# Optimization experiments

Measured on AMD Instinct MI355X. Metric: run time of the kernel, lower is better.

## Reference

```python
import jax, jax.numpy as jnp
import numpy as np

N_NODES = 50000


def gcn_conv(x, W, b, row, col, num_nodes):
    """PyG-style GCNConv: out = D^{-1/2}(A+I)D^{-1/2} (x @ W) + b.

    row/col already include self-loops. x: [N, Fin], W: [Fin, Fout].
    """
    h = x @ W  # [N, Fout]
    deg = jax.ops.segment_sum(jnp.ones_like(col, dtype=h.dtype), col,
                              num_segments=num_nodes)  # in-degree incl. self-loop
    dinv = jnp.where(deg > 0, jax.lax.rsqrt(deg), 0.0)
    norm = dinv[row] * dinv[col]  # [E]
    msgs = h[row] * norm[:, None]  # gather + scale, [E, Fout]
    out = jax.ops.segment_sum(msgs, col, num_segments=num_nodes)  # scatter-add
    return out + b


def setup_inputs() -> dict:
    key = jax.random.key(0)
    k1, k2, k3, k4 = jax.random.split(key, 4)
    Fin, Fh, Fout = 128, 128, 64
    E = 800000
    x = jax.random.normal(k1, (N_NODES, Fin), dtype=jnp.float32)
    edge_index = jax.random.randint(k2, (2, E), 0, N_NODES, dtype=jnp.int64)
    # Glorot-ish init for weights
    W1 = jax.random.normal(k3, (Fin, Fh), dtype=jnp.float32) / np.sqrt(Fin)
    b1 = jnp.zeros((Fh,), dtype=jnp.float32)
    W2 = jax.random.normal(k4, (Fh, Fout), dtype=jnp.float32) / np.sqrt(Fh)
    b2 = jnp.zeros((Fout,), dtype=jnp.float32)
    return {"x": x, "edge_index": edge_index, "W1": W1, "b1": b1,
            "W2": W2, "b2": b2}


def reference(x, edge_index, W1, b1, W2, b2):
    n = x.shape[0]
    # add self-loops once (shared by both conv layers)
    loops = jnp.arange(n, dtype=edge_index.dtype)
    row = jnp.concatenate([edge_index[0], loops])
    col = jnp.concatenate([edge_index[1], loops])
    h = jax.nn.relu(gcn_conv(x, W1, b1, row, col, n))
    # dropout(p=0.5) is identity in eval mode (self.training == False)
    return gcn_conv(h, W2, b2, row, col, n)
```

## Files before the change

kernel.cpp:

```cpp
#include <hip/hip_runtime.h>


constexpr int KD = 128;
constexpr int CHUNK = 2048;
constexpr int BCAP = 6144;

using short8  = __attribute__((ext_vector_type(8))) short;
using float4v = __attribute__((ext_vector_type(4))) float;
using uint4v  = __attribute__((ext_vector_type(4))) unsigned int;


__device__ __forceinline__ unsigned short f2bf(float f) {
    unsigned int u = __float_as_uint(f);
    u = (u + 0x7fffu + ((u >> 16) & 1u)) >> 16;
    return (unsigned short)u;
}

__device__ __forceinline__ float2 bfpair(unsigned int u) {
    float2 f;
    f.x = __uint_as_float(u << 16);
    f.y = __uint_as_float(u & 0xffff0000u);
    return f;
}

__device__ __forceinline__ unsigned int packbf(float x, float y) {
    return (unsigned int)f2bf(x) | ((unsigned int)f2bf(y) << 16);
}

__device__ __forceinline__ void bfsplit(float x, unsigned short& h, unsigned short& l) {
    h = f2bf(x);
    float fh = __uint_as_float((unsigned int)h << 16);
    l = f2bf(x - fh);
}

__global__ __launch_bounds__(256) void scatter_setup(
        const int* __restrict__ row, const int* __restrict__ col,
        int* gcur, unsigned int* __restrict__ bpack, int E, int NBS,
        const float* __restrict__ W1, unsigned short* __restrict__ Wth1,
        unsigned short* __restrict__ Wtl1,
        const float* __restrict__ W2, unsigned short* __restrict__ Wth2,
        unsigned short* __restrict__ Wtl2) {
    __shared__ int lh[256];
    __shared__ int lbase[256];

    if ((int)blockIdx.x >= NBS) {
        int id = ((int)blockIdx.x - NBS) * 256 + threadIdx.x;
        unsigned short h, l;
        if (id < 16384) {
            int k = id >> 7, n = id & 127;
            bfsplit(W1[id], h, l);
            Wth1[n * KD + k] = h;
            Wtl1[n * KD + k] = l;
        } else {
            int id2 = id - 16384;
            int k = id2 >> 6, n = id2 & 63;
            bfsplit(W2[id2], h, l);
            Wth2[n * KD + k] = h;
            Wtl2[n * KD + k] = l;
        }
        return;
    }

    lh[threadIdx.x] = 0;
    __syncthreads();
    int base = (int)blockIdx.x * CHUNK;
#pragma unroll
    for (int r = 0; r < CHUNK / 256; ++r) {
        int e = base + r * 256 + threadIdx.x;
        if (e < E) atomicAdd(&lh[col[e] >> 8], 1);
    }
    __syncthreads();
    int c0 = lh[threadIdx.x];
    lbase[threadIdx.x] = c0 ? (threadIdx.x * BCAP + atomicAdd(&gcur[threadIdx.x], c0)) : 0;
    __syncthreads();
    lh[threadIdx.x] = 0;
    __syncthreads();
#pragma unroll
    for (int r = 0; r < CHUNK / 256; ++r) {
        int e = base + r * 256 + threadIdx.x;
        if (e < E) {
            int c = col[e];
            int b = c >> 8;
            int slot = lbase[b] + atomicAdd(&lh[b], 1);
            bpack[slot] = ((unsigned int)row[e] << 16) | (unsigned int)c;
        }
    }
}

__global__ __launch_bounds__(256) void csr_and_gemm1(
        const unsigned int* __restrict__ bpack, const int* __restrict__ gcur,
        int* __restrict__ rowptr, float* __restrict__ dinv,
        unsigned short* __restrict__ srow, int N, int E, int NBUCKET,
        const float* __restrict__ X,
        const unsigned short* __restrict__ Wth,
        const unsigned short* __restrict__ Wtl,
        unsigned short* __restrict__ G) {
    __shared__ int s[256];
    __shared__ int lh[256];
    __shared__ int lcur[256];
    __shared__ int sh_bstart;

    if ((int)blockIdx.x < NBUCKET) {
        int b = blockIdx.x;
        int t = threadIdx.x;
        int cntb = gcur[t];
        s[t] = cntb;
        __syncthreads();
        for (int off = 1; off < 256; off <<= 1) {
            int tv = (t >= off) ? s[t - off] : 0;
            __syncthreads();
            s[t] += tv;
            __syncthreads();
        }
        if (t == b) sh_bstart = s[t] - cntb;
        if (b == 0 && t == 0) rowptr[N] = E;
        lh[t] = 0;
        __syncthreads();
        int bstart = sh_bstart;
        int nE = gcur[b];
        int base = b * BCAP;
        for (int i = t; i < nE; i += 256)
            atomicAdd(&lh[bpack[base + i] & 255], 1);
        __syncthreads();
        int v = lh[t];
        s[t] = v;
        __syncthreads();
        for (int off = 1; off < 256; off <<= 1) {
            int tv = (t >= off) ? s[t - off] : 0;
            __syncthreads();
            s[t] += tv;
            __syncthreads();
        }
        int myStart = bstart + s[t] - v;
        int node = (b << 8) + t;
        if (node < N) {
            rowptr[node] = myStart;
            dinv[node] = rsqrtf(1.0f + (float)v);
        }
        lcur[t] = myStart;
        __syncthreads();
        for (int i = t; i < nE; i += 256) {
            unsigned int p = bpack[base + i];
            int slot = atomicAdd(&lcur[p & 255], 1);
            srow[slot] = (unsigned short)(p >> 16);
        }
    } else {
        constexpr int FOUT = 128, NT = 8;
        int wave = threadIdx.x >> 6;
        int lane = threadIdx.x & 63;
        int row0 = (((int)blockIdx.x - NBUCKET) * 4 + wave) * 16;
        if (row0 >= N) return;
        int m = lane & 15;
        int quad = lane >> 4;

        float4v acc[NT];
#pragma unroll
        for (int ct = 0; ct < NT; ++ct) acc[ct] = (float4v){0.f, 0.f, 0.f, 0.f};

        const float* xrow = X + (size_t)(row0 + m) * KD + quad * 8;

#pragma unroll
        for (int ks = 0; ks < 4; ++ks) {
            float4 xa = *(const float4*)(xrow + ks * 32);
            float4 xb = *(const float4*)(xrow + ks * 32 + 4);
            float xs[8] = {xa.x, xa.y, xa.z, xa.w, xb.x, xb.y, xb.z, xb.w};
            short8 ah, al;
#pragma unroll
            for (int j = 0; j < 8; ++j) {
                unsigned short h, l;
                bfsplit(xs[j], h, l);
                ah[j] = (short)h;
                al[j] = (short)l;
            }
            int koff = ks * 32 + quad * 8;
#pragma unroll
            for (int ct = 0; ct < NT; ++ct) {
                short8 bh = *(const short8*)(Wth + (size_t)(ct * 16 + m) * KD + koff);
                short8 bl = *(const short8*)(Wtl + (size_t)(ct * 16 + m) * KD + koff);
                acc[ct] = __builtin_amdgcn_mfma_f32_16x16x32_bf16(ah, bh, acc[ct], 0, 0, 0);
                acc[ct] = __builtin_amdgcn_mfma_f32_16x16x32_bf16(al, bh, acc[ct], 0, 0, 0);
                acc[ct] = __builtin_amdgcn_mfma_f32_16x16x32_bf16(ah, bl, acc[ct], 0, 0, 0);
            }
        }

#pragma unroll
        for (int r = 0; r < 4; ++r) {
            int row = row0 + quad * 4 + r;
#pragma unroll
            for (int ct = 0; ct < NT; ++ct) {
                G[(size_t)row * FOUT + ct * 16 + m] = f2bf(acc[ct][r]);
            }
        }
    }
}

__global__ __launch_bounds__(256) void gather128_gemm2(
        const int* __restrict__ rowptr,
        const unsigned short* __restrict__ srow,
        const unsigned int* __restrict__ G,
        const float* __restrict__ dinv,
        const float* __restrict__ bias,
        const unsigned short* __restrict__ Wth,
        const unsigned short* __restrict__ Wtl,
        unsigned short* __restrict__ G2,
        int N, int E) {
    __shared__ unsigned int lhs[16 * 64];
    __shared__ float ldinv[16];

    int lane = threadIdx.x & 63;
    int l16 = threadIdx.x & 15;
    int q = threadIdx.x >> 4;
    int node = (int)blockIdx.x * 16 + q;
    bool valid = node < N;
    int nc = valid ? node : 0;
    int beg = rowptr[nc];
    int end = rowptr[nc + 1];
    int deg = valid ? (end - beg) : 0;
    float dn = dinv[nc];
    if (l16 == 0) ldinv[q] = dn;

    const uint4v* Gv = (const uint4v*)G;

    uint4v s0 = Gv[(size_t)nc * 16 + l16];
    float ac[8];
    {
        float2 v0 = bfpair(s0[0]), v1 = bfpair(s0[1]);
        float2 v2 = bfpair(s0[2]), v3 = bfpair(s0[3]);
        ac[0] = v0.x * dn; ac[1] = v0.y * dn;
        ac[2] = v1.x * dn; ac[3] = v1.y * dn;
        ac[4] = v2.x * dn; ac[5] = v2.y * dn;
        ac[6] = v3.x * dn; ac[7] = v3.y * dn;
    }

    int dm = max(deg, __shfl_xor(deg, 16));
    dm = max(dm, __shfl_xor(dm, 32));

    for (int w = 0; w < dm; w += 16) {
        int li = w + l16;
        li = (li < deg) ? li : (deg > 0 ? deg - 1 : 0);
        li += beg;
        li = (li < E) ? li : (E - 1);
        int rv = (int)srow[li];
        float dv = dinv[rv];
        int lim = dm - w;
        for (int g = 0; g < 16 && g < lim; g += 4) {
            uint4v u[4];
            float dr[4];
#pragma unroll
            for (int j = 0; j < 4; ++j) {
                int src = (lane & 48) | (g + j);
                int r = __shfl(rv, src);
                dr[j] = __shfl(dv, src);
                u[j] = Gv[(size_t)r * 16 + l16];
            }
            float s[8] = {0.f, 0.f, 0.f, 0.f, 0.f, 0.f, 0.f, 0.f};
#pragma unroll
            for (int j = 0; j < 4; ++j) {
                bool ok = (w + g + j) < deg;
#pragma unroll
                for (int c = 0; c < 4; ++c) {
                    unsigned int uv = ok ? u[j][c] : 0u;
                    float2 v = bfpair(uv);
                    s[2 * c]     = fmaf(dr[j], v.x, s[2 * c]);
                    s[2 * c + 1] = fmaf(dr[j], v.y, s[2 * c + 1]);
                }
            }
#pragma unroll
            for (int c = 0; c < 8; ++c) ac[c] += s[c];
        }
    }

    {
        float4 bv0 = ((const float4*)bias)[l16 * 2];
        float4 bv1 = ((const float4*)bias)[l16 * 2 + 1];
        float o[8];
        o[0] = ac[0] * dn + bv0.x; o[1] = ac[1] * dn + bv0.y;
        o[2] = ac[2] * dn + bv0.z; o[3] = ac[3] * dn + bv0.w;
        o[4] = ac[4] * dn + bv1.x; o[5] = ac[5] * dn + bv1.y;
        o[6] = ac[6] * dn + bv1.z; o[7] = ac[7] * dn + bv1.w;
#pragma unroll
        for (int c = 0; c < 8; ++c) o[c] = fmaxf(o[c], 0.f);
        int lb = q * 64 + l16 * 4;
        lhs[lb + 0] = packbf(o[0], o[1]);
        lhs[lb + 1] = packbf(o[2], o[3]);
        lhs[lb + 2] = packbf(o[4], o[5]);
        lhs[lb + 3] = packbf(o[6], o[7]);
    }
    __syncthreads();

    int ct = threadIdx.x >> 6;
    int m = lane & 15;
    int quad = lane >> 4;

    float4v acc = (float4v){0.f, 0.f, 0.f, 0.f};
#pragma unroll
    for (int ks = 0; ks < 4; ++ks) {
        short8 a = *(const short8*)&lhs[m * 64 + ks * 16 + quad * 4];
        int koff = ks * 32 + quad * 8;
        short8 bh = *(const short8*)(Wth + (size_t)(ct * 16 + m) * KD + koff);
        short8 bl = *(const short8*)(Wtl + (size_t)(ct * 16 + m) * KD + koff);
        acc = __builtin_amdgcn_mfma_f32_16x16x32_bf16(a, bh, acc, 0, 0, 0);
        acc = __builtin_amdgcn_mfma_f32_16x16x32_bf16(a, bl, acc, 0, 0, 0);
    }

#pragma unroll
    for (int r = 0; r < 4; ++r) {
        int rr = quad * 4 + r;
        int gnode = (int)blockIdx.x * 16 + rr;
        if (gnode < N) {
            G2[(size_t)gnode * 64 + ct * 16 + m] = f2bf(acc[r] * ldinv[rr]);
        }
    }
}

template <bool RELU>
__global__ __launch_bounds__(256) void gather64(const int* __restrict__ rowptr,
                                                const unsigned short* __restrict__ srow,
                                                const unsigned int* __restrict__ G,
                                                const float* __restrict__ dinv,
                                                const float* __restrict__ bias,
                                                float* __restrict__ O, int N, int E) {
    int tid = blockIdx.x * 256 + (int)threadIdx.x;
    int node = tid >> 4;
    int lane = threadIdx.x & 63;
    int l16 = lane & 15;
    bool valid = node < N;
    int nc = valid ? node : (N - 1);
    int beg = rowptr[nc];
    int end = rowptr[nc + 1];
    int deg = valid ? (end - beg) : 0;

    uint2 s0 = ((const uint2*)G)[(size_t)nc * 16 + l16];
    float2 p0 = bfpair(s0.x), p1 = bfpair(s0.y);
    float ax = p0.x, ay = p0.y, az = p1.x, aw = p1.y;

    int dm = max(deg, __shfl_xor(deg, 16));
    dm = max(dm, __shfl_xor(dm, 32));

    for (int w = 0; w < dm; w += 16) {
        int li = w + l16;
        li = (li < deg) ? li : (deg > 0 ? deg - 1 : 0);
        li += beg;
        li = (li < E) ? li : (E - 1);
        int rv = (int)srow[li];
        int lim = dm - w;
        for (int g = 0; g < 16 && g < lim; g += 8) {
            uint2 u[8];
#pragma unroll
            for (int j = 0; j < 8; ++j) {
                int src = (lane & 48) | (g + j);
                int r = __shfl(rv, src);
                u[j] = ((const uint2*)G)[(size_t)r * 16 + l16];
            }
            float sx = 0.f, sy = 0.f, sz = 0.f, sw = 0.f;
#pragma unroll
            for (int j = 0; j < 8; ++j) {
                bool ok = (w + g + j) < deg;
                unsigned int ux = ok ? u[j].x : 0u;
                unsigned int uy = ok ? u[j].y : 0u;
                float2 v0 = bfpair(ux), v1 = bfpair(uy);
                sx += v0.x; sy += v0.y; sz += v1.x; sw += v1.y;
            }
            ax += sx; ay += sy; az += sz; aw += sw;
        }
    }
    if (!valid) return;
    float s = dinv[nc];
    float4 bv = ((const float4*)bias)[l16];
    float ox = ax * s + bv.x;
    float oy = ay * s + bv.y;
    float oz = az * s + bv.z;
    float ow = aw * s + bv.w;
    if (RELU) {
        ox = fmaxf(ox, 0.f); oy = fmaxf(oy, 0.f);
        oz = fmaxf(oz, 0.f); ow = fmaxf(ow, 0.f);
    }
    float4v o = {ox, oy, oz, ow};
    __builtin_nontemporal_store(o, (float4v*)O + (size_t)nc * 16 + l16);
}

extern "C" void kernel_launch(void* const* d_in, const int* in_sizes, int n_in,
                              void* d_out, int out_size, void* d_ws, size_t ws_size,
                              hipStream_t stream) {
    const float* x  = (const float*)d_in[0];
    const int*   ei = (const int*)d_in[1];
    const float* W1 = (const float*)d_in[2];
    const float* b1 = (const float*)d_in[3];
    const float* W2 = (const float*)d_in[4];
    const float* b2 = (const float*)d_in[5];
    float* out = (float*)d_out;

    int N = in_sizes[0] / 128;
    int E = in_sizes[1] / 2;
    const int* row = ei;
    const int* col = ei + E;

    char* ws = (char*)d_ws;
    float* dinv   = (float*)(ws + 0x000000);
    int*   rowptr = (int*)  (ws + 0x080000);
    int*   gcur   = (int*)  (ws + 0x0F9000);
    unsigned short* srow = (unsigned short*)(ws + 0x100000);
    unsigned short* g1 = (unsigned short*)(ws + 0x440000);
    unsigned short* wth1 = (unsigned short*)(ws + 0x10C0000);
    unsigned short* wtl1 = (unsigned short*)(ws + 0x10D0000);
    unsigned short* wth2 = (unsigned short*)(ws + 0x10E0000);
    unsigned short* wtl2 = (unsigned short*)(ws + 0x10F0000);
    unsigned int* bpack = (unsigned int*)(ws + 0x1200000);
    unsigned short* g2 = (unsigned short*)(ws + 0x2C00000);

    int NB_BKT  = (E + CHUNK - 1) / CHUNK;
    int NBUCKET = (N + 255) / 256;
    int NB_GEMM1 = (N + 63) / 64;
    int NB_SETUP = 96;

    hipMemsetAsync(gcur, 0, 256 * sizeof(int), stream);
    scatter_setup<<<NB_BKT + NB_SETUP, 256, 0, stream>>>(
        row, col, gcur, bpack, E, NB_BKT, W1, wth1, wtl1, W2, wth2, wtl2);
    csr_and_gemm1<<<NBUCKET + NB_GEMM1, 256, 0, stream>>>(
        bpack, gcur, rowptr, dinv, srow, N, E, NBUCKET, x, wth1, wtl1, g1);

    int nb;
    nb = (N + 15) / 16;
    gather128_gemm2<<<nb, 256, 0, stream>>>(rowptr, srow, (const unsigned int*)g1,
                                            dinv, b1, wth2, wtl2, g2, N, E);

    nb = (N + 15) / 16;
    gather64<false><<<nb, 256, 0, stream>>>(rowptr, srow, (const unsigned int*)g2,
                                            dinv, b2, out, N, E);
}
```

Measured before the change: 182.6 us.

## Split neighbor lists by source-node range and gather 64 nodes per block

```diff
diff --git a/kernel.cpp b/kernel.cpp
--- a/kernel.cpp
+++ b/kernel.cpp
@@ -89,15 +89,15 @@
 
 __global__ __launch_bounds__(256) void csr_and_gemm1(
         const unsigned int* __restrict__ bpack, const int* __restrict__ gcur,
-        int* __restrict__ rowptr, float* __restrict__ dinv,
+        int* __restrict__ rowptrS, float* __restrict__ dinv,
         unsigned short* __restrict__ srow, int N, int E, int NBUCKET,
         const float* __restrict__ X,
         const unsigned short* __restrict__ Wth,
         const unsigned short* __restrict__ Wtl,
         unsigned short* __restrict__ G) {
     __shared__ int s[256];
-    __shared__ int lh[256];
-    __shared__ int lcur[256];
+    __shared__ int lh[1024];
+    __shared__ int lcur[1024];
     __shared__ int sh_bstart;
 
     if ((int)blockIdx.x < NBUCKET) {
@@ -113,16 +113,20 @@
             __syncthreads();
         }
         if (t == b) sh_bstart = s[t] - cntb;
-        if (b == 0 && t == 0) rowptr[N] = E;
-        lh[t] = 0;
+        if (b == 0 && t == 0) rowptrS[4 * N] = E;
+#pragma unroll
+        for (int k = 0; k < 4; ++k) lh[t * 4 + k] = 0;
         __syncthreads();
         int bstart = sh_bstart;
         int nE = gcur[b];
         int base = b * BCAP;
-        for (int i = t; i < nE; i += 256)
-            atomicAdd(&lh[bpack[base + i] & 255], 1);
-        __syncthreads();
-        int v = lh[t];
+        for (int i = t; i < nE; i += 256) {
+            unsigned int p = bpack[base + i];
+            atomicAdd(&lh[(p & 255) * 4 + (p >> 30)], 1);
+        }
+        __syncthreads();
+        int e0 = lh[t * 4], e1 = lh[t * 4 + 1], e2 = lh[t * 4 + 2], e3 = lh[t * 4 + 3];
+        int v = e0 + e1 + e2 + e3;
         s[t] = v;
         __syncthreads();
         for (int off = 1; off < 256; off <<= 1) {
@@ -134,14 +138,20 @@
         int myStart = bstart + s[t] - v;
         int node = (b << 8) + t;
         if (node < N) {
-            rowptr[node] = myStart;
+            rowptrS[node * 4 + 0] = myStart;
+            rowptrS[node * 4 + 1] = myStart + e0;
+            rowptrS[node * 4 + 2] = myStart + e0 + e1;
+            rowptrS[node * 4 + 3] = myStart + e0 + e1 + e2;
             dinv[node] = rsqrtf(1.0f + (float)v);
         }
-        lcur[t] = myStart;
+        lcur[t * 4 + 0] = myStart;
+        lcur[t * 4 + 1] = myStart + e0;
+        lcur[t * 4 + 2] = myStart + e0 + e1;
+        lcur[t * 4 + 3] = myStart + e0 + e1 + e2;
         __syncthreads();
         for (int i = t; i < nE; i += 256) {
             unsigned int p = bpack[base + i];
-            int slot = atomicAdd(&lcur[p & 255], 1);
+            int slot = atomicAdd(&lcur[(p & 255) * 4 + (p >> 30)], 1);
             srow[slot] = (unsigned short)(p >> 16);
         }
     } else {
@@ -194,8 +204,8 @@
     }
 }
 
-__global__ __launch_bounds__(256) void gather128_gemm2(
-        const int* __restrict__ rowptr,
+__global__ __launch_bounds__(256, 4) void gather128_gemm2_seg(
+        const int* __restrict__ rowptrS,
         const unsigned short* __restrict__ srow,
         const unsigned int* __restrict__ G,
         const float* __restrict__ dinv,
@@ -208,113 +218,126 @@
     __shared__ float ldinv[16];
 
     int lane = threadIdx.x & 63;
-    int l16 = threadIdx.x & 15;
-    int q = threadIdx.x >> 4;
-    int node = (int)blockIdx.x * 16 + q;
-    bool valid = node < N;
-    int nc = valid ? node : 0;
-    int beg = rowptr[nc];
-    int end = rowptr[nc + 1];
-    int deg = valid ? (end - beg) : 0;
-    float dn = dinv[nc];
-    if (l16 == 0) ldinv[q] = dn;
-
+    int l16  = threadIdx.x & 15;
+    int q    = threadIdx.x >> 4;
     const uint4v* Gv = (const uint4v*)G;
 
-    uint4v s0 = Gv[(size_t)nc * 16 + l16];
-    float ac[8];
-    {
+    float acc[4][8];
+    float dns[4];
+
+#pragma unroll
+    for (int t = 0; t < 4; ++t) {
+        int node = (int)blockIdx.x * 64 + t * 16 + q;
+        int nc = (node < N) ? node : 0;
+        float dn = dinv[nc];
+        dns[t] = dn;
+        uint4v s0 = Gv[(size_t)nc * 16 + l16];
         float2 v0 = bfpair(s0[0]), v1 = bfpair(s0[1]);
         float2 v2 = bfpair(s0[2]), v3 = bfpair(s0[3]);
-        ac[0] = v0.x * dn; ac[1] = v0.y * dn;
-        ac[2] = v1.x * dn; ac[3] = v1.y * dn;
-        ac[4] = v2.x * dn; ac[5] = v2.y * dn;
-        ac[6] = v3.x * dn; ac[7] = v3.y * dn;
-    }
-
-    int dm = max(deg, __shfl_xor(deg, 16));
-    dm = max(dm, __shfl_xor(dm, 32));
-
-    for (int w = 0; w < dm; w += 16) {
-        int li = w + l16;
-        li = (li < deg) ? li : (deg > 0 ? deg - 1 : 0);
-        li += beg;
-        li = (li < E) ? li : (E - 1);
-        int rv = (int)srow[li];
-        float dv = dinv[rv];
-        int lim = dm - w;
-        for (int g = 0; g < 16 && g < lim; g += 4) {
-            uint4v u[4];
-            float dr[4];
-#pragma unroll
-            for (int j = 0; j < 4; ++j) {
-                int src = (lane & 48) | (g + j);
-                int r = __shfl(rv, src);
-                dr[j] = __shfl(dv, src);
-                u[j] = Gv[(size_t)r * 16 + l16];
-            }
-            float s[8] = {0.f, 0.f, 0.f, 0.f, 0.f, 0.f, 0.f, 0.f};
-#pragma unroll
-            for (int j = 0; j < 4; ++j) {
-                bool ok = (w + g + j) < deg;
-#pragma unroll
-                for (int c = 0; c < 4; ++c) {
-                    unsigned int uv = ok ? u[j][c] : 0u;
-                    float2 v = bfpair(uv);
-                    s[2 * c]     = fmaf(dr[j], v.x, s[2 * c]);
-                    s[2 * c + 1] = fmaf(dr[j], v.y, s[2 * c + 1]);
+        acc[t][0] = v0.x * dn; acc[t][1] = v0.y * dn;
+        acc[t][2] = v1.x * dn; acc[t][3] = v1.y * dn;
+        acc[t][4] = v2.x * dn; acc[t][5] = v2.y * dn;
+        acc[t][6] = v3.x * dn; acc[t][7] = v3.y * dn;
+    }
+
+    for (int sgm = 0; sgm < 4; ++sgm) {
+#pragma unroll
+        for (int t = 0; t < 4; ++t) {
+            int node = (int)blockIdx.x * 64 + t * 16 + q;
+            bool valid = node < N;
+            int nc = valid ? node : 0;
+            int beg = rowptrS[nc * 4 + sgm];
+            int end = rowptrS[nc * 4 + sgm + 1];
+            int deg = valid ? (end - beg) : 0;
+            int dm = max(deg, __shfl_xor(deg, 16));
+            dm = max(dm, __shfl_xor(dm, 32));
+            for (int w = 0; w < dm; w += 16) {
+                int li = w + l16;
+                li = (li < deg) ? li : (deg > 0 ? deg - 1 : 0);
+                li += beg;
+                li = (li < E) ? li : (E - 1);
+                int rv = (int)srow[li];
+                float dv = dinv[rv];
+                int lim = dm - w;
+                for (int g = 0; g < 16 && g < lim; g += 4) {
+                    uint4v u[4];
+                    float dr[4];
+#pragma unroll
+                    for (int j = 0; j < 4; ++j) {
+                        int src = (lane & 48) | (g + j);
+                        int r = __shfl(rv, src);
+                        dr[j] = __shfl(dv, src);
+                        u[j] = Gv[(size_t)r * 16 + l16];
+                    }
+                    float sa[8] = {0.f, 0.f, 0.f, 0.f, 0.f, 0.f, 0.f, 0.f};
+#pragma unroll
+                    for (int j = 0; j < 4; ++j) {
+                        bool ok = (w + g + j) < deg;
+#pragma unroll
+                        for (int c = 0; c < 4; ++c) {
+                            unsigned int uv = ok ? u[j][c] : 0u;
+                            float2 v = bfpair(uv);
+                            sa[2 * c]     = fmaf(dr[j], v.x, sa[2 * c]);
+                            sa[2 * c + 1] = fmaf(dr[j], v.y, sa[2 * c + 1]);
+                        }
+                    }
+#pragma unroll
+                    for (int c = 0; c < 8; ++c) acc[t][c] += sa[c];
                 }
             }
-#pragma unroll
-            for (int c = 0; c < 8; ++c) ac[c] += s[c];
-        }
-    }
-
-    {
-        float4 bv0 = ((const float4*)bias)[l16 * 2];
-        float4 bv1 = ((const float4*)bias)[l16 * 2 + 1];
-        float o[8];
-        o[0] = ac[0] * dn + bv0.x; o[1] = ac[1] * dn + bv0.y;
-        o[2] = ac[2] * dn + bv0.z; o[3] = ac[3] * dn + bv0.w;
-        o[4] = ac[4] * dn + bv1.x; o[5] = ac[5] * dn + bv1.y;
-        o[6] = ac[6] * dn + bv1.z; o[7] = ac[7] * dn + bv1.w;
-#pragma unroll
-        for (int c = 0; c < 8; ++c) o[c] = fmaxf(o[c], 0.f);
-        int lb = q * 64 + l16 * 4;
-        lhs[lb + 0] = packbf(o[0], o[1]);
-        lhs[lb + 1] = packbf(o[2], o[3]);
-        lhs[lb + 2] = packbf(o[4], o[5]);
-        lhs[lb + 3] = packbf(o[6], o[7]);
-    }
-    __syncthreads();
-
-    int ct = threadIdx.x >> 6;
-    int m = lane & 15;
-    int quad = lane >> 4;
-
-    float4v acc = (float4v){0.f, 0.f, 0.f, 0.f};
-#pragma unroll
-    for (int ks = 0; ks < 4; ++ks) {
-        short8 a = *(const short8*)&lhs[m * 64 + ks * 16 + quad * 4];
-        int koff = ks * 32 + quad * 8;
-        short8 bh = *(const short8*)(Wth + (size_t)(ct * 16 + m) * KD + koff);
-        short8 bl = *(const short8*)(Wtl + (size_t)(ct * 16 + m) * KD + koff);
-        acc = __builtin_amdgcn_mfma_f32_16x16x32_bf16(a, bh, acc, 0, 0, 0);
-        acc = __builtin_amdgcn_mfma_f32_16x16x32_bf16(a, bl, acc, 0, 0, 0);
-    }
-
-#pragma unroll
-    for (int r = 0; r < 4; ++r) {
-        int rr = quad * 4 + r;
-        int gnode = (int)blockIdx.x * 16 + rr;
-        if (gnode < N) {
-            G2[(size_t)gnode * 64 + ct * 16 + m] = f2bf(acc[r] * ldinv[rr]);
-        }
+        }
+    }
+
+#pragma unroll
+    for (int t = 0; t < 4; ++t) {
+        {
+            float dn = dns[t];
+            if (l16 == 0) ldinv[q] = dn;
+            float4 bv0 = ((const float4*)bias)[l16 * 2];
+            float4 bv1 = ((const float4*)bias)[l16 * 2 + 1];
+            float o[8];
+            o[0] = acc[t][0] * dn + bv0.x; o[1] = acc[t][1] * dn + bv0.y;
+            o[2] = acc[t][2] * dn + bv0.z; o[3] = acc[t][3] * dn + bv0.w;
+            o[4] = acc[t][4] * dn + bv1.x; o[5] = acc[t][5] * dn + bv1.y;
+            o[6] = acc[t][6] * dn + bv1.z; o[7] = acc[t][7] * dn + bv1.w;
+#pragma unroll
+            for (int c = 0; c < 8; ++c) o[c] = fmaxf(o[c], 0.f);
+            int lb = q * 64 + l16 * 4;
+            lhs[lb + 0] = packbf(o[0], o[1]);
+            lhs[lb + 1] = packbf(o[2], o[3]);
+            lhs[lb + 2] = packbf(o[4], o[5]);
+            lhs[lb + 3] = packbf(o[6], o[7]);
+        }
+        __syncthreads();
+        {
+            int ct = threadIdx.x >> 6;
+            int m = lane & 15;
+            int quad = lane >> 4;
+            float4v fa = (float4v){0.f, 0.f, 0.f, 0.f};
+#pragma unroll
+            for (int ks = 0; ks < 4; ++ks) {
+                short8 a = *(const short8*)&lhs[m * 64 + ks * 16 + quad * 4];
+                int koff = ks * 32 + quad * 8;
+                short8 bh = *(const short8*)(Wth + (size_t)(ct * 16 + m) * KD + koff);
+                short8 bl = *(const short8*)(Wtl + (size_t)(ct * 16 + m) * KD + koff);
+                fa = __builtin_amdgcn_mfma_f32_16x16x32_bf16(a, bh, fa, 0, 0, 0);
+                fa = __builtin_amdgcn_mfma_f32_16x16x32_bf16(a, bl, fa, 0, 0, 0);
+            }
+#pragma unroll
+            for (int r = 0; r < 4; ++r) {
+                int rr = quad * 4 + r;
+                int gnode = (int)blockIdx.x * 64 + t * 16 + rr;
+                if (gnode < N) {
+                    G2[(size_t)gnode * 64 + ct * 16 + m] = f2bf(fa[r] * ldinv[rr]);
+                }
+            }
+        }
+        __syncthreads();
     }
 }
 
 template <bool RELU>
-__global__ __launch_bounds__(256) void gather64(const int* __restrict__ rowptr,
+__global__ __launch_bounds__(256) void gather64(const int* __restrict__ rowptrS,
                                                 const unsigned short* __restrict__ srow,
                                                 const unsigned int* __restrict__ G,
                                                 const float* __restrict__ dinv,
@@ -326,8 +349,8 @@
     int l16 = lane & 15;
     bool valid = node < N;
     int nc = valid ? node : (N - 1);
-    int beg = rowptr[nc];
-    int end = rowptr[nc + 1];
+    int beg = rowptrS[nc * 4];
+    int end = rowptrS[nc * 4 + 4];
     int deg = valid ? (end - beg) : 0;
 
     uint2 s0 = ((const uint2*)G)[(size_t)nc * 16 + l16];
@@ -396,10 +419,10 @@
     const int* col = ei + E;
 
     char* ws = (char*)d_ws;
-    float* dinv   = (float*)(ws + 0x000000);
-    int*   rowptr = (int*)  (ws + 0x080000);
-    int*   gcur   = (int*)  (ws + 0x0F9000);
-    unsigned short* srow = (unsigned short*)(ws + 0x100000);
+    float* dinv    = (float*)(ws + 0x000000);
+    int*   rowptrS = (int*)  (ws + 0x080000);
+    int*   gcur    = (int*)  (ws + 0x150000);
+    unsigned short* srow = (unsigned short*)(ws + 0x160000);
     unsigned short* g1 = (unsigned short*)(ws + 0x440000);
     unsigned short* wth1 = (unsigned short*)(ws + 0x10C0000);
     unsigned short* wtl1 = (unsigned short*)(ws + 0x10D0000);
@@ -417,14 +440,15 @@
     scatter_setup<<<NB_BKT + NB_SETUP, 256, 0, stream>>>(
         row, col, gcur, bpack, E, NB_BKT, W1, wth1, wtl1, W2, wth2, wtl2);
     csr_and_gemm1<<<NBUCKET + NB_GEMM1, 256, 0, stream>>>(
-        bpack, gcur, rowptr, dinv, srow, N, E, NBUCKET, x, wth1, wtl1, g1);
+        bpack, gcur, rowptrS, dinv, srow, N, E, NBUCKET, x, wth1, wtl1, g1);
 
     int nb;
+    nb = (N + 63) / 64;
+    gather128_gemm2_seg<<<nb, 256, 0, stream>>>(rowptrS, srow,
+                                                (const unsigned int*)g1,
+                                                dinv, b1, wth2, wtl2, g2, N, E);
+
     nb = (N + 15) / 16;
-    gather128_gemm2<<<nb, 256, 0, stream>>>(rowptr, srow, (const unsigned int*)g1,
-                                            dinv, b1, wth2, wtl2, g2, N, E);
-
-    nb = (N + 15) / 16;
-    gather64<false><<<nb, 256, 0, stream>>>(rowptr, srow, (const unsigned int*)g2,
+    gather64<false><<<nb, 256, 0, stream>>>(rowptrS, srow, (const unsigned int*)g2,
                                             dinv, b2, out, N, E);
 }
```

Measured after the change: 191.2 us. +4.7%, slower.
